# Kernel optimization log

Measured on AMD Instinct MI355X. Metric: run time of the kernel, lower is better.

Reference implementation:

```python
import jax, jax.numpy as jnp
import numpy as np

N = 50000
E = 1600000
IN_C = 64
HID = 16
HEADS = 4
OUT_C = 1
ATT_SLOPE = 0.2   # GATConv negative_slope for attention logits
ACT_SLOPE = 0.01  # F.leaky_relu default between layers


def _glorot(key, shape):
    fan_in, fan_out = shape[0], shape[-1]
    lim = jnp.sqrt(6.0 / (fan_in + fan_out))
    return jax.random.uniform(key, shape, jnp.float32, -lim, lim)


def setup_inputs() -> dict:
    key = jax.random.key(0)
    ks = jax.random.split(key, 12)
    x = jax.random.normal(ks[0], (N, IN_C), jnp.float32)
    edge_index = jax.random.randint(ks[1], (2, E), 0, N, jnp.int64)
    return {
        "x": x,
        "edge_index": edge_index,
        # GAT layer 1: in -> HID per head, HEADS heads (concat)
        "W1": _glorot(ks[2], (IN_C, HEADS * HID)),
        "att_src1": _glorot(ks[3], (HEADS, HID)),
        "att_dst1": _glorot(ks[4], (HEADS, HID)),
        "b1": jnp.zeros((HEADS * HID,), jnp.float32),
        # GAT layer 2: HEADS*HID -> HID, 1 head
        "W2": _glorot(ks[5], (HEADS * HID, HID)),
        "att_src2": _glorot(ks[6], (1, HID)),
        "att_dst2": _glorot(ks[7], (1, HID)),
        "b2": jnp.zeros((HID,), jnp.float32),
        # final linear
        "Wo": _glorot(ks[8], (HID, OUT_C)),
        "bo": jnp.zeros((OUT_C,), jnp.float32),
    }


def _gat_layer(x, src, dst, W, a_src, a_dst, b, n_nodes):
    """PyG GATConv (eval mode): h = xW; edge logits from additive attention;
    segment softmax over incoming edges of each dst; weighted scatter-sum."""
    H, C = a_src.shape
    h = (x @ W).reshape(n_nodes, H, C)                       # [N, H, C]
    alpha_s = jnp.einsum("nhc,hc->nh", h, a_src)             # [N, H]
    alpha_d = jnp.einsum("nhc,hc->nh", h, a_dst)             # [N, H]
    e = jax.nn.leaky_relu(alpha_s[src] + alpha_d[dst], ATT_SLOPE)  # [E, H]
    m = jax.ops.segment_max(e, dst, num_segments=n_nodes)    # [N, H]
    w = jnp.exp(e - m[dst])
    denom = jax.ops.segment_sum(w, dst, num_segments=n_nodes)
    alpha = w / denom[dst]                                   # [E, H] (self-loops => denom>0)
    out = jax.ops.segment_sum(h[src] * alpha[:, :, None], dst, num_segments=n_nodes)
    return out.reshape(n_nodes, H * C) + b                   # concat heads + bias


def reference(x, edge_index, W1, att_src1, att_dst1, b1,
              W2, att_src2, att_dst2, b2, Wo, bo):
    n = x.shape[0]
    loops = jnp.arange(n, dtype=edge_index.dtype)
    src = jnp.concatenate([edge_index[0], loops])            # add_self_loops=True
    dst = jnp.concatenate([edge_index[1], loops])
    h = _gat_layer(x, src, dst, W1, att_src1, att_dst1, b1, n)
    h = jax.nn.leaky_relu(h, ACT_SLOPE)
    h = _gat_layer(h, src, dst, W2, att_src2, att_dst2, b2, n)
    h = jax.nn.leaky_relu(h, ACT_SLOPE)
    return h @ Wo + bo                                       # [N, 1]
```

## Files before the change

kernel.cpp:

```cpp
#include <hip/hip_runtime.h>
#include <hip/hip_bf16.h>
#include <cstdint>

#define N_NODES 50000
#define N_EDGES 1600000
#define EE (N_EDGES + N_NODES)
#define BSH 5
#define BSIZE 32
#define NBUCKET ((N_NODES + BSIZE - 1) >> BSH)
#define CSH 11
#define CAP 2048
#define BIN_BLOCKS 403
#define GEMM_BLOCKS 3125

__device__ __forceinline__ float lrelu(float x, float s) { return x >= 0.f ? x : s * x; }
__device__ __forceinline__ float bflo(uint32_t v) { return __uint_as_float(v << 16); }
__device__ __forceinline__ float bfhi(uint32_t v) { return __uint_as_float(v & 0xFFFF0000u); }
__device__ __forceinline__ uint32_t packbf(float a, float b) {
    uint32_t ua = __float_as_uint(a), ub = __float_as_uint(b);
    ua += 0x7FFF + ((ua >> 16) & 1);
    ub += 0x7FFF + ((ub >> 16) & 1);
    return (ua >> 16) | (ub & 0xFFFF0000u);
}
__device__ __forceinline__ float rdlane(float v, int l) {
    return __uint_as_float(__builtin_amdgcn_readlane(__float_as_uint(v), l));
}

__global__ __launch_bounds__(256) void k_pre(
    const float* __restrict__ x, const float* __restrict__ W1,
    const float* __restrict__ as_w, const float* __restrict__ ad_w,
    uint32_t* __restrict__ h1b, float* __restrict__ as1, float* __restrict__ ad1,
    const int* __restrict__ src, const int* __restrict__ dst,
    int* __restrict__ bcur, uint32_t* __restrict__ binned) {
    if (blockIdx.x < BIN_BLOCKS) {
        __shared__ int lcnt[NBUCKET];
        __shared__ int lbase[NBUCKET];
        const int T = 16;
        for (int i = threadIdx.x; i < NBUCKET; i += 256) lcnt[i] = 0;
        __syncthreads();
        uint32_t pv[T];
        uint32_t pm[T];
        int base = blockIdx.x * (256 * T);
        if (base + 256 * T <= N_EDGES) {
            const int4* s4 = (const int4*)(src + base);
            const int4* d4 = (const int4*)(dst + base);
#pragma unroll
            for (int k = 0; k < 4; k++) {
                int4 sv = s4[threadIdx.x + k * 256];
                int4 dv = d4[threadIdx.x + k * 256];
                int ss[4] = {sv.x, sv.y, sv.z, sv.w};
                int dd[4] = {dv.x, dv.y, dv.z, dv.w};
#pragma unroll
                for (int j = 0; j < 4; j++) {
                    int b = dd[j] >> BSH;
                    int r = atomicAdd(&lcnt[b], 1);
                    pv[k * 4 + j] = (uint32_t)ss[j] | ((uint32_t)(dd[j] & (BSIZE - 1)) << 16);
                    pm[k * 4 + j] = (uint32_t)r | ((uint32_t)b << 16);
                }
            }
        } else {
#pragma unroll
            for (int k = 0; k < T; k++) {
                int e = base + ((k & 3) * 4 + (k >> 2)) * 256 + threadIdx.x;
                pm[k] = 0xFFFFFFFFu;
                if (e < EE) {
                    int s, d;
                    if (e < N_EDGES) { s = src[e]; d = dst[e]; } else { s = e - N_EDGES; d = s; }
                    int b = d >> BSH;
                    int r = atomicAdd(&lcnt[b], 1);
                    pv[k] = (uint32_t)s | ((uint32_t)(d & (BSIZE - 1)) << 16);
                    pm[k] = (uint32_t)r | ((uint32_t)b << 16);
                }
            }
        }
        __syncthreads();
        for (int i = threadIdx.x; i < NBUCKET; i += 256) {
            int c = lcnt[i];
            if (c) lbase[i] = atomicAdd(&bcur[i], c);
        }
        __syncthreads();
#pragma unroll
        for (int k = 0; k < T; k++) {
            if (pm[k] != 0xFFFFFFFFu) {
                int b = pm[k] >> 16, r = pm[k] & 0xFFFF;
                binned[((size_t)b << CSH) + lbase[b] + r] = pv[k];
            }
        }
        return;
    }
    int c = threadIdx.x & 63;
    int wv = threadIdx.x >> 6;
    float wreg[64];
#pragma unroll
    for (int k = 0; k < 64; k++) wreg[k] = W1[k * 64 + c];
    float aw = as_w[c];
    float dw = ad_w[c];
    int base = (blockIdx.x - BIN_BLOCKS) * 16 + wv * 4;
#pragma unroll
    for (int r = 0; r < 4; r++) {
        int n = base + r;
        float xr = x[n * 64 + c];
        float a0 = 0.f, a1 = 0.f, a2 = 0.f, a3 = 0.f;
#pragma unroll
        for (int k = 0; k < 64; k += 4) {
            a0 = fmaf(rdlane(xr, k),     wreg[k],     a0);
            a1 = fmaf(rdlane(xr, k + 1), wreg[k + 1], a1);
            a2 = fmaf(rdlane(xr, k + 2), wreg[k + 2], a2);
            a3 = fmaf(rdlane(xr, k + 3), wreg[k + 3], a3);
        }
        float acc = (a0 + a1) + (a2 + a3);
        float other = __shfl_xor(acc, 1, 64);
        if (!(c & 1)) h1b[n * 32 + (c >> 1)] = packbf(acc, other);
        float asv = acc * aw;
        float adv = acc * dw;
#pragma unroll
        for (int off = 1; off < 16; off <<= 1) {
            asv += __shfl_xor(asv, off, 64);
            adv += __shfl_xor(adv, off, 64);
        }
        if ((c & 15) == 0) { as1[n * 4 + (c >> 4)] = asv; ad1[n * 4 + (c >> 4)] = adv; }
    }
}

__global__ __launch_bounds__(256) void kB_sort_aggr1(
    const int* __restrict__ bcur, const uint32_t* __restrict__ binned,
    int* __restrict__ rowdesc, unsigned short* __restrict__ esrc,
    const float* __restrict__ as1, const float* __restrict__ ad1,
    const uint32_t* __restrict__ h1b,
    const float* __restrict__ b1, const float* __restrict__ W2,
    const float* __restrict__ as2w, const float* __restrict__ ad2w,
    float* __restrict__ h2, float* __restrict__ as2, float* __restrict__ ad2) {
    int b = blockIdx.x, tid = threadIdx.x, wv = tid >> 6;
    int p0 = b << CSH;
    int L = bcur[b];
    __shared__ int cnt4[4][BSIZE];
    __shared__ int wbase[4][BSIZE];
    __shared__ int sdesc[BSIZE];
    __shared__ unsigned short sesrc[CAP + 16];
    for (int i = tid; i < 4 * BSIZE; i += 256) ((int*)cnt4)[i] = 0;
    __syncthreads();

    uint32_t pv[8];
    unsigned short rk[8];
#pragma unroll
    for (int k = 0; k < 8; k++) {
        int i = tid + k * 256;
        if (i < L) {
            uint32_t v = binned[p0 + i];
            pv[k] = v;
            rk[k] = (unsigned short)atomicAdd(&cnt4[wv][(v >> 16) & (BSIZE - 1)], 1);
        }
    }
    __syncthreads();

    if (tid < BSIZE) {
        int tot = cnt4[0][tid] + cnt4[1][tid] + cnt4[2][tid] + cnt4[3][tid];
        int incl = tot;
#pragma unroll
        for (int off = 1; off < BSIZE; off <<= 1) {
            int t = __shfl_up(incl, off, BSIZE);
            if ((tid & (BSIZE - 1)) >= off) incl += t;
        }
        int excl = incl - tot;
        int node = (b << BSH) + tid;
        int d = excl | (tot << 13);
        sdesc[tid] = d;
        if (node < N_NODES) rowdesc[node] = d;
        int wb = excl;
#pragma unroll
        for (int w = 0; w < 4; w++) { wbase[w][tid] = wb; wb += cnt4[w][tid]; }
    }
    __syncthreads();

#pragma unroll
    for (int k = 0; k < 8; k++) {
        int i = tid + k * 256;
        if (i < L) {
            uint32_t v = pv[k];
            int dl = (v >> 16) & (BSIZE - 1);
            sesrc[wbase[wv][dl] + (int)rk[k]] = (unsigned short)(v & 0xFFFF);
        }
    }
    __syncthreads();

    for (int i = tid; i < L; i += 256) esrc[p0 + i] = sesrc[i];

    int lane = tid & 63;
    int slot = lane >> 3, cl = lane & 7;
    int hc = cl >> 1;
    const uint4* h1b4 = (const uint4*)h1b;
    float4 bb0 = *(const float4*)(b1 + 8 * cl);
    float4 bb1 = *(const float4*)(b1 + 8 * cl + 4);
    int co = lane & 15, kg = lane >> 4;
    int l0 = 2 * kg, l1 = 2 * kg + 1;
    const float* w2r = W2 + (16 * kg) * 16 + co;
    float asw = as2w[co], adw = ad2w[co];

    for (int nn = 0; nn < 8; nn++) {
        int ln = (wv << 3) + nn;
        int n = (b << BSH) + ln;
        if (n >= N_NODES) break;
        int md = sdesc[ln];
        int begin = md & (CAP - 1);
        int deg = md >> 13;
        float ad1h = ad1[n * 4 + hc];

        float a0 = 0.f, a1 = 0.f, a2 = 0.f, a3 = 0.f, a4 = 0.f, a5 = 0.f, a6 = 0.f, a7 = 0.f, dsum = 0.f;
        int iters = (deg + 7) >> 3;
#pragma unroll 4
        for (int it = 0; it < iters; it++) {
            int idx = it * 8 + slot;
            bool ok = idx < deg;
            int s = ok ? (int)sesrc[begin + idx] : 0;
            float e = as1[s * 4 + hc] + ad1h;
            float w = __expf(e >= 0.f ? e : 0.2f * e);
            w = ok ? w : 0.f;
            uint4 v = h1b4[s * 8 + cl];
            dsum += w;
            a0 += w * bflo(v.x); a1 += w * bfhi(v.x);
            a2 += w * bflo(v.y); a3 += w * bfhi(v.y);
            a4 += w * bflo(v.z); a5 += w * bfhi(v.z);
            a6 += w * bflo(v.w); a7 += w * bfhi(v.w);
        }
#pragma unroll
        for (int off = 8; off <= 32; off <<= 1) {
            a0 += __shfl_xor(a0, off, 64); a1 += __shfl_xor(a1, off, 64);
            a2 += __shfl_xor(a2, off, 64); a3 += __shfl_xor(a3, off, 64);
            a4 += __shfl_xor(a4, off, 64); a5 += __shfl_xor(a5, off, 64);
            a6 += __shfl_xor(a6, off, 64); a7 += __shfl_xor(a7, off, 64);
            dsum += __shfl_xor(dsum, off, 64);
        }
        float dinv = 1.f / dsum;

        float act0 = lrelu(a0 * dinv + bb0.x, 0.01f);
        float act1 = lrelu(a1 * dinv + bb0.y, 0.01f);
        float act2 = lrelu(a2 * dinv + bb0.z, 0.01f);
        float act3 = lrelu(a3 * dinv + bb0.w, 0.01f);
        float act4 = lrelu(a4 * dinv + bb1.x, 0.01f);
        float act5 = lrelu(a5 * dinv + bb1.y, 0.01f);
        float act6 = lrelu(a6 * dinv + bb1.z, 0.01f);
        float act7 = lrelu(a7 * dinv + bb1.w, 0.01f);

        float g = 0.f;
        g = fmaf(__shfl(act0, l0, 64), w2r[0 * 16],  g);
        g = fmaf(__shfl(act1, l0, 64), w2r[1 * 16],  g);
        g = fmaf(__shfl(act2, l0, 64), w2r[2 * 16],  g);
        g = fmaf(__shfl(act3, l0, 64), w2r[3 * 16],  g);
        g = fmaf(__shfl(act4, l0, 64), w2r[4 * 16],  g);
        g = fmaf(__shfl(act5, l0, 64), w2r[5 * 16],  g);
        g = fmaf(__shfl(act6, l0, 64), w2r[6 * 16],  g);
        g = fmaf(__shfl(act7, l0, 64), w2r[7 * 16],  g);
        g = fmaf(__shfl(act0, l1, 64), w2r[8 * 16],  g);
        g = fmaf(__shfl(act1, l1, 64), w2r[9 * 16],  g);
        g = fmaf(__shfl(act2, l1, 64), w2r[10 * 16], g);
        g = fmaf(__shfl(act3, l1, 64), w2r[11 * 16], g);
        g = fmaf(__shfl(act4, l1, 64), w2r[12 * 16], g);
        g = fmaf(__shfl(act5, l1, 64), w2r[13 * 16], g);
        g = fmaf(__shfl(act6, l1, 64), w2r[14 * 16], g);
        g = fmaf(__shfl(act7, l1, 64), w2r[15 * 16], g);
        g += __shfl_xor(g, 16, 64);
        g += __shfl_xor(g, 32, 64);
        if (lane < 16) h2[n * 16 + co] = g;
        float asv = g * asw;
        float adv2 = g * adw;
#pragma unroll
        for (int off = 1; off < 16; off <<= 1) {
            asv += __shfl_xor(asv, off, 64);
            adv2 += __shfl_xor(adv2, off, 64);
        }
        if (lane == 0) { as2[n] = asv; ad2[n] = adv2; }
    }
}

__global__ __launch_bounds__(256) void k_aggr2(
    const int* __restrict__ rowdesc, const unsigned short* __restrict__ esrc,
    const float* __restrict__ as2, const float* __restrict__ ad2,
    const float* __restrict__ h2,
    const float* __restrict__ b2, const float* __restrict__ Wo,
    const float* __restrict__ bo, float* __restrict__ out) {
    int n = blockIdx.x * 4 + (threadIdx.x >> 6);
    int lane = threadIdx.x & 63;
    int md = rowdesc[n];
    int begin = ((n >> BSH) << CSH) + (md & (CAP - 1));
    int deg = md >> 13;
    float adv = ad2[n];

    int slot = lane >> 3, c2 = lane & 7;
    const float2* h22 = (const float2*)h2;
    float acc0 = 0.f, acc1 = 0.f, dsum = 0.f;

    int iters = (deg + 7) >> 3;
#pragma unroll 4
    for (int it = 0; it < iters; it++) {
        int idx = it * 8 + slot;
        bool ok = idx < deg;
        int s = ok ? (int)esrc[begin + idx] : 0;
        float e = as2[s] + adv;
        float w = __expf(e >= 0.f ? e : 0.2f * e);
        w = ok ? w : 0.f;
        float2 hv = h22[s * 8 + c2];
        acc0 += w * hv.x;
        acc1 += w * hv.y;
        dsum += w;
    }
#pragma unroll
    for (int off = 8; off <= 32; off <<= 1) {
        acc0 += __shfl_xor(acc0, off, 64);
        acc1 += __shfl_xor(acc1, off, 64);
        dsum += __shfl_xor(dsum, off, 64);
    }
    float v0 = lrelu(acc0 / dsum + b2[2 * c2], 0.01f) * Wo[2 * c2];
    float v1 = lrelu(acc1 / dsum + b2[2 * c2 + 1], 0.01f) * Wo[2 * c2 + 1];
    float y = v0 + v1;
    y += __shfl_xor(y, 1, 64);
    y += __shfl_xor(y, 2, 64);
    y += __shfl_xor(y, 4, 64);
    if (lane == 0) out[n] = y + bo[0];
}

extern "C" void kernel_launch(void* const* d_in, const int* in_sizes, int n_in,
                              void* d_out, int out_size, void* d_ws, size_t ws_size,
                              hipStream_t stream) {
    const float* x    = (const float*)d_in[0];
    const int*   ei   = (const int*)d_in[1];
    const float* W1   = (const float*)d_in[2];
    const float* as1w = (const float*)d_in[3];
    const float* ad1w = (const float*)d_in[4];
    const float* b1   = (const float*)d_in[5];
    const float* W2   = (const float*)d_in[6];
    const float* as2w = (const float*)d_in[7];
    const float* ad2w = (const float*)d_in[8];
    const float* b2   = (const float*)d_in[9];
    const float* Wo   = (const float*)d_in[10];
    const float* bo   = (const float*)d_in[11];
    float* out = (float*)d_out;

    const int* srcp = ei;
    const int* dstp = ei + N_EDGES;

    char* p = (char*)d_ws;
    auto alloc = [&](size_t bytes) -> char* {
        char* r = p;
        p += (bytes + 255) / 256 * 256;
        return r;
    };
    int*            bcur    = (int*)alloc((size_t)(NBUCKET + 1) * 4);
    int*            rowdesc = (int*)alloc((size_t)N_NODES * 4);
    uint32_t*       binned  = (uint32_t*)alloc((size_t)NBUCKET * CAP * 4);
    unsigned short* esrc    = (unsigned short*)alloc((size_t)NBUCKET * CAP * 2 + 256);
    float*          h2      = (float*)alloc((size_t)N_NODES * 16 * 4);
    uint32_t*       h1b     = (uint32_t*)alloc((size_t)N_NODES * 32 * 4);
    float*          as1     = (float*)alloc((size_t)N_NODES * 4 * 4);
    float*          ad1     = (float*)alloc((size_t)N_NODES * 4 * 4);
    float*          as2     = (float*)alloc((size_t)N_NODES * 4);
    float*          ad2     = (float*)alloc((size_t)N_NODES * 4);
    (void)alloc(4 * 1024 * 1024);

    hipMemsetAsync(bcur, 0, (size_t)(NBUCKET + 1) * 4, stream);

    k_pre<<<BIN_BLOCKS + GEMM_BLOCKS, 256, 0, stream>>>(x, W1, as1w, ad1w, h1b, as1, ad1,
                                                        srcp, dstp, bcur, binned);
    kB_sort_aggr1<<<NBUCKET, 256, 0, stream>>>(bcur, binned, rowdesc, esrc,
                                               as1, ad1, h1b, b1, W2, as2w, ad2w, h2, as2, ad2);
    k_aggr2<<<N_NODES / 4, 256, 0, stream>>>(rowdesc, esrc, as2, ad2, h2, b2, Wo, bo, out);
}
```

Measured before the change: 193.7 us.

## Split fused sort+aggregate kernel, store layer-2 features in bf16, halve bin chunk

The fused per-bucket sort and layer-1 aggregation kernel is split into a sort-only kernel and a separate per-node aggregation kernel that runs one wave per node across 12500 blocks. Before, only about 1563 blocks did that aggregation, each wave walking 8 nodes in sequence. Layer-2 node features are now stored as packed bf16, halving the bytes gathered per edge in the second aggregation at some precision cost. The edge-binning chunk per block is also halved, doubling the number of binning blocks. The split adds one kernel launch and a round trip of the sorted edge list through global memory.

```diff
diff --git a/kernel.cpp b/kernel.cpp
--- a/kernel.cpp
+++ b/kernel.cpp
@@ -10,7 +10,8 @@
 #define NBUCKET ((N_NODES + BSIZE - 1) >> BSH)
 #define CSH 11
 #define CAP 2048
-#define BIN_BLOCKS 403
+#define BIN_CHUNK 2048
+#define BIN_BLOCKS ((EE + BIN_CHUNK - 1) / BIN_CHUNK)
 #define GEMM_BLOCKS 3125
 
 __device__ __forceinline__ float lrelu(float x, float s) { return x >= 0.f ? x : s * x; }
@@ -35,17 +36,17 @@
     if (blockIdx.x < BIN_BLOCKS) {
         __shared__ int lcnt[NBUCKET];
         __shared__ int lbase[NBUCKET];
-        const int T = 16;
+        const int T = 8;
         for (int i = threadIdx.x; i < NBUCKET; i += 256) lcnt[i] = 0;
         __syncthreads();
         uint32_t pv[T];
         uint32_t pm[T];
-        int base = blockIdx.x * (256 * T);
-        if (base + 256 * T <= N_EDGES) {
+        int base = blockIdx.x * BIN_CHUNK;
+        if (base + BIN_CHUNK <= N_EDGES) {
             const int4* s4 = (const int4*)(src + base);
             const int4* d4 = (const int4*)(dst + base);
 #pragma unroll
-            for (int k = 0; k < 4; k++) {
+            for (int k = 0; k < 2; k++) {
                 int4 sv = s4[threadIdx.x + k * 256];
                 int4 dv = d4[threadIdx.x + k * 256];
                 int ss[4] = {sv.x, sv.y, sv.z, sv.w};
@@ -59,9 +60,8 @@
                 }
             }
         } else {
-#pragma unroll
             for (int k = 0; k < T; k++) {
-                int e = base + ((k & 3) * 4 + (k >> 2)) * 256 + threadIdx.x;
+                int e = base + k * 256 + threadIdx.x;
                 pm[k] = 0xFFFFFFFFu;
                 if (e < EE) {
                     int s, d;
@@ -122,21 +122,14 @@
     }
 }
 
-__global__ __launch_bounds__(256) void kB_sort_aggr1(
-    const int* __restrict__ bcur, const uint32_t* __restrict__ binned,
-    int* __restrict__ rowdesc, unsigned short* __restrict__ esrc,
-    const float* __restrict__ as1, const float* __restrict__ ad1,
-    const uint32_t* __restrict__ h1b,
-    const float* __restrict__ b1, const float* __restrict__ W2,
-    const float* __restrict__ as2w, const float* __restrict__ ad2w,
-    float* __restrict__ h2, float* __restrict__ as2, float* __restrict__ ad2) {
+__global__ __launch_bounds__(256) void kB_sort(const int* __restrict__ bcur, const uint32_t* __restrict__ binned,
+                                               int* __restrict__ rowdesc, unsigned short* __restrict__ esrc) {
     int b = blockIdx.x, tid = threadIdx.x, wv = tid >> 6;
     int p0 = b << CSH;
     int L = bcur[b];
     __shared__ int cnt4[4][BSIZE];
     __shared__ int wbase[4][BSIZE];
-    __shared__ int sdesc[BSIZE];
-    __shared__ unsigned short sesrc[CAP + 16];
+    __shared__ unsigned short sesrc[CAP];
     for (int i = tid; i < 4 * BSIZE; i += 256) ((int*)cnt4)[i] = 0;
     __syncthreads();
 
@@ -163,9 +156,7 @@
         }
         int excl = incl - tot;
         int node = (b << BSH) + tid;
-        int d = excl | (tot << 13);
-        sdesc[tid] = d;
-        if (node < N_NODES) rowdesc[node] = d;
+        if (node < N_NODES) rowdesc[node] = excl | (tot << 13);
         int wb = excl;
 #pragma unroll
         for (int w = 0; w < 4; w++) { wbase[w][tid] = wb; wb += cnt4[w][tid]; }
@@ -184,98 +175,103 @@
     __syncthreads();
 
     for (int i = tid; i < L; i += 256) esrc[p0 + i] = sesrc[i];
-
-    int lane = tid & 63;
+}
+
+__global__ __launch_bounds__(256) void k_aggr1f(
+    const int* __restrict__ rowdesc, const unsigned short* __restrict__ esrc,
+    const float* __restrict__ as1, const float* __restrict__ ad1,
+    const uint32_t* __restrict__ h1b,
+    const float* __restrict__ b1, const float* __restrict__ W2,
+    const float* __restrict__ as2w, const float* __restrict__ ad2w,
+    uint32_t* __restrict__ h2b, float* __restrict__ as2, float* __restrict__ ad2) {
+    int n = blockIdx.x * 4 + (threadIdx.x >> 6);
+    int lane = threadIdx.x & 63;
+    int md = rowdesc[n];
+    int begin = ((n >> BSH) << CSH) + (md & (CAP - 1));
+    int deg = md >> 13;
+
     int slot = lane >> 3, cl = lane & 7;
     int hc = cl >> 1;
+    float ad1h = ad1[n * 4 + hc];
+
     const uint4* h1b4 = (const uint4*)h1b;
+    float a0 = 0.f, a1 = 0.f, a2 = 0.f, a3 = 0.f, a4 = 0.f, a5 = 0.f, a6 = 0.f, a7 = 0.f, dsum = 0.f;
+
+    int iters = (deg + 7) >> 3;
+#pragma unroll 4
+    for (int it = 0; it < iters; it++) {
+        int idx = it * 8 + slot;
+        bool ok = idx < deg;
+        int s = ok ? (int)esrc[begin + idx] : 0;
+        float e = as1[s * 4 + hc] + ad1h;
+        float w = __expf(e >= 0.f ? e : 0.2f * e);
+        w = ok ? w : 0.f;
+        uint4 v = h1b4[s * 8 + cl];
+        dsum += w;
+        a0 += w * bflo(v.x); a1 += w * bfhi(v.x);
+        a2 += w * bflo(v.y); a3 += w * bfhi(v.y);
+        a4 += w * bflo(v.z); a5 += w * bfhi(v.z);
+        a6 += w * bflo(v.w); a7 += w * bfhi(v.w);
+    }
+#pragma unroll
+    for (int off = 8; off <= 32; off <<= 1) {
+        a0 += __shfl_xor(a0, off, 64); a1 += __shfl_xor(a1, off, 64);
+        a2 += __shfl_xor(a2, off, 64); a3 += __shfl_xor(a3, off, 64);
+        a4 += __shfl_xor(a4, off, 64); a5 += __shfl_xor(a5, off, 64);
+        a6 += __shfl_xor(a6, off, 64); a7 += __shfl_xor(a7, off, 64);
+        dsum += __shfl_xor(dsum, off, 64);
+    }
+    float dinv = 1.f / dsum;
+
     float4 bb0 = *(const float4*)(b1 + 8 * cl);
     float4 bb1 = *(const float4*)(b1 + 8 * cl + 4);
+    float act0 = lrelu(a0 * dinv + bb0.x, 0.01f);
+    float act1 = lrelu(a1 * dinv + bb0.y, 0.01f);
+    float act2 = lrelu(a2 * dinv + bb0.z, 0.01f);
+    float act3 = lrelu(a3 * dinv + bb0.w, 0.01f);
+    float act4 = lrelu(a4 * dinv + bb1.x, 0.01f);
+    float act5 = lrelu(a5 * dinv + bb1.y, 0.01f);
+    float act6 = lrelu(a6 * dinv + bb1.z, 0.01f);
+    float act7 = lrelu(a7 * dinv + bb1.w, 0.01f);
+
     int co = lane & 15, kg = lane >> 4;
     int l0 = 2 * kg, l1 = 2 * kg + 1;
     const float* w2r = W2 + (16 * kg) * 16 + co;
-    float asw = as2w[co], adw = ad2w[co];
-
-    for (int nn = 0; nn < 8; nn++) {
-        int ln = (wv << 3) + nn;
-        int n = (b << BSH) + ln;
-        if (n >= N_NODES) break;
-        int md = sdesc[ln];
-        int begin = md & (CAP - 1);
-        int deg = md >> 13;
-        float ad1h = ad1[n * 4 + hc];
-
-        float a0 = 0.f, a1 = 0.f, a2 = 0.f, a3 = 0.f, a4 = 0.f, a5 = 0.f, a6 = 0.f, a7 = 0.f, dsum = 0.f;
-        int iters = (deg + 7) >> 3;
-#pragma unroll 4
-        for (int it = 0; it < iters; it++) {
-            int idx = it * 8 + slot;
-            bool ok = idx < deg;
-            int s = ok ? (int)sesrc[begin + idx] : 0;
-            float e = as1[s * 4 + hc] + ad1h;
-            float w = __expf(e >= 0.f ? e : 0.2f * e);
-            w = ok ? w : 0.f;
-            uint4 v = h1b4[s * 8 + cl];
-            dsum += w;
-            a0 += w * bflo(v.x); a1 += w * bfhi(v.x);
-            a2 += w * bflo(v.y); a3 += w * bfhi(v.y);
-            a4 += w * bflo(v.z); a5 += w * bfhi(v.z);
-            a6 += w * bflo(v.w); a7 += w * bfhi(v.w);
-        }
-#pragma unroll
-        for (int off = 8; off <= 32; off <<= 1) {
-            a0 += __shfl_xor(a0, off, 64); a1 += __shfl_xor(a1, off, 64);
-            a2 += __shfl_xor(a2, off, 64); a3 += __shfl_xor(a3, off, 64);
-            a4 += __shfl_xor(a4, off, 64); a5 += __shfl_xor(a5, off, 64);
-            a6 += __shfl_xor(a6, off, 64); a7 += __shfl_xor(a7, off, 64);
-            dsum += __shfl_xor(dsum, off, 64);
-        }
-        float dinv = 1.f / dsum;
-
-        float act0 = lrelu(a0 * dinv + bb0.x, 0.01f);
-        float act1 = lrelu(a1 * dinv + bb0.y, 0.01f);
-        float act2 = lrelu(a2 * dinv + bb0.z, 0.01f);
-        float act3 = lrelu(a3 * dinv + bb0.w, 0.01f);
-        float act4 = lrelu(a4 * dinv + bb1.x, 0.01f);
-        float act5 = lrelu(a5 * dinv + bb1.y, 0.01f);
-        float act6 = lrelu(a6 * dinv + bb1.z, 0.01f);
-        float act7 = lrelu(a7 * dinv + bb1.w, 0.01f);
-
-        float g = 0.f;
-        g = fmaf(__shfl(act0, l0, 64), w2r[0 * 16],  g);
-        g = fmaf(__shfl(act1, l0, 64), w2r[1 * 16],  g);
-        g = fmaf(__shfl(act2, l0, 64), w2r[2 * 16],  g);
-        g = fmaf(__shfl(act3, l0, 64), w2r[3 * 16],  g);
-        g = fmaf(__shfl(act4, l0, 64), w2r[4 * 16],  g);
-        g = fmaf(__shfl(act5, l0, 64), w2r[5 * 16],  g);
-        g = fmaf(__shfl(act6, l0, 64), w2r[6 * 16],  g);
-        g = fmaf(__shfl(act7, l0, 64), w2r[7 * 16],  g);
-        g = fmaf(__shfl(act0, l1, 64), w2r[8 * 16],  g);
-        g = fmaf(__shfl(act1, l1, 64), w2r[9 * 16],  g);
-        g = fmaf(__shfl(act2, l1, 64), w2r[10 * 16], g);
-        g = fmaf(__shfl(act3, l1, 64), w2r[11 * 16], g);
-        g = fmaf(__shfl(act4, l1, 64), w2r[12 * 16], g);
-        g = fmaf(__shfl(act5, l1, 64), w2r[13 * 16], g);
-        g = fmaf(__shfl(act6, l1, 64), w2r[14 * 16], g);
-        g = fmaf(__shfl(act7, l1, 64), w2r[15 * 16], g);
-        g += __shfl_xor(g, 16, 64);
-        g += __shfl_xor(g, 32, 64);
-        if (lane < 16) h2[n * 16 + co] = g;
-        float asv = g * asw;
-        float adv2 = g * adw;
-#pragma unroll
-        for (int off = 1; off < 16; off <<= 1) {
-            asv += __shfl_xor(asv, off, 64);
-            adv2 += __shfl_xor(adv2, off, 64);
-        }
-        if (lane == 0) { as2[n] = asv; ad2[n] = adv2; }
-    }
+    float g = 0.f;
+    g = fmaf(__shfl(act0, l0, 64), w2r[0 * 16],  g);
+    g = fmaf(__shfl(act1, l0, 64), w2r[1 * 16],  g);
+    g = fmaf(__shfl(act2, l0, 64), w2r[2 * 16],  g);
+    g = fmaf(__shfl(act3, l0, 64), w2r[3 * 16],  g);
+    g = fmaf(__shfl(act4, l0, 64), w2r[4 * 16],  g);
+    g = fmaf(__shfl(act5, l0, 64), w2r[5 * 16],  g);
+    g = fmaf(__shfl(act6, l0, 64), w2r[6 * 16],  g);
+    g = fmaf(__shfl(act7, l0, 64), w2r[7 * 16],  g);
+    g = fmaf(__shfl(act0, l1, 64), w2r[8 * 16],  g);
+    g = fmaf(__shfl(act1, l1, 64), w2r[9 * 16],  g);
+    g = fmaf(__shfl(act2, l1, 64), w2r[10 * 16], g);
+    g = fmaf(__shfl(act3, l1, 64), w2r[11 * 16], g);
+    g = fmaf(__shfl(act4, l1, 64), w2r[12 * 16], g);
+    g = fmaf(__shfl(act5, l1, 64), w2r[13 * 16], g);
+    g = fmaf(__shfl(act6, l1, 64), w2r[14 * 16], g);
+    g = fmaf(__shfl(act7, l1, 64), w2r[15 * 16], g);
+    g += __shfl_xor(g, 16, 64);
+    g += __shfl_xor(g, 32, 64);
+    float godd = __shfl_xor(g, 1, 64);
+    if (lane < 16 && !(lane & 1)) h2b[n * 8 + (lane >> 1)] = packbf(g, godd);
+    float asv = g * as2w[co];
+    float adv2 = g * ad2w[co];
+#pragma unroll
+    for (int off = 1; off < 16; off <<= 1) {
+        asv += __shfl_xor(asv, off, 64);
+        adv2 += __shfl_xor(adv2, off, 64);
+    }
+    if (lane == 0) { as2[n] = asv; ad2[n] = adv2; }
 }
 
 __global__ __launch_bounds__(256) void k_aggr2(
     const int* __restrict__ rowdesc, const unsigned short* __restrict__ esrc,
     const float* __restrict__ as2, const float* __restrict__ ad2,
-    const float* __restrict__ h2,
+    const uint32_t* __restrict__ h2b,
     const float* __restrict__ b2, const float* __restrict__ Wo,
     const float* __restrict__ bo, float* __restrict__ out) {
     int n = blockIdx.x * 4 + (threadIdx.x >> 6);
@@ -286,7 +282,6 @@
     float adv = ad2[n];
 
     int slot = lane >> 3, c2 = lane & 7;
-    const float2* h22 = (const float2*)h2;
     float acc0 = 0.f, acc1 = 0.f, dsum = 0.f;
 
     int iters = (deg + 7) >> 3;
@@ -298,9 +293,9 @@
         float e = as2[s] + adv;
         float w = __expf(e >= 0.f ? e : 0.2f * e);
         w = ok ? w : 0.f;
-        float2 hv = h22[s * 8 + c2];
-        acc0 += w * hv.x;
-        acc1 += w * hv.y;
+        uint32_t hv = h2b[s * 8 + c2];
+        acc0 += w * bflo(hv);
+        acc1 += w * bfhi(hv);
         dsum += w;
     }
 #pragma unroll
@@ -348,19 +343,19 @@
     int*            rowdesc = (int*)alloc((size_t)N_NODES * 4);
     uint32_t*       binned  = (uint32_t*)alloc((size_t)NBUCKET * CAP * 4);
     unsigned short* esrc    = (unsigned short*)alloc((size_t)NBUCKET * CAP * 2 + 256);
-    float*          h2      = (float*)alloc((size_t)N_NODES * 16 * 4);
+    uint32_t*       h2b     = (uint32_t*)alloc((size_t)N_NODES * 8 * 4);
     uint32_t*       h1b     = (uint32_t*)alloc((size_t)N_NODES * 32 * 4);
     float*          as1     = (float*)alloc((size_t)N_NODES * 4 * 4);
     float*          ad1     = (float*)alloc((size_t)N_NODES * 4 * 4);
     float*          as2     = (float*)alloc((size_t)N_NODES * 4);
     float*          ad2     = (float*)alloc((size_t)N_NODES * 4);
-    (void)alloc(4 * 1024 * 1024);
 
     hipMemsetAsync(bcur, 0, (size_t)(NBUCKET + 1) * 4, stream);
 
     k_pre<<<BIN_BLOCKS + GEMM_BLOCKS, 256, 0, stream>>>(x, W1, as1w, ad1w, h1b, as1, ad1,
                                                         srcp, dstp, bcur, binned);
-    kB_sort_aggr1<<<NBUCKET, 256, 0, stream>>>(bcur, binned, rowdesc, esrc,
-                                               as1, ad1, h1b, b1, W2, as2w, ad2w, h2, as2, ad2);
-    k_aggr2<<<N_NODES / 4, 256, 0, stream>>>(rowdesc, esrc, as2, ad2, h2, b2, Wo, bo, out);
-}
+    kB_sort<<<NBUCKET, 256, 0, stream>>>(bcur, binned, rowdesc, esrc);
+    k_aggr1f<<<N_NODES / 4, 256, 0, stream>>>(rowdesc, esrc, as1, ad1, h1b, b1, W2, as2w, ad2w,
+                                              h2b, as2, ad2);
+    k_aggr2<<<N_NODES / 4, 256, 0, stream>>>(rowdesc, esrc, as2, ad2, h2b, b2, Wo, bo, out);
+}
```

Result: slower. 205.7 us (+6.2%).
